# Optimization experiments

Hardware: AMD Instinct MI355X
Metric: run time of the kernel (lower is better)

Reference implementation:

```python
import jax, jax.numpy as jnp
import numpy as np

VOC = 32000
D = 512          # embedding_dim == hidden_dim
POS = 1024       # position_embeddings_count


def _layernorm(x, gamma, beta, eps=1e-5):
    mu = jnp.mean(x, axis=-1, keepdims=True)
    var = jnp.var(x, axis=-1, keepdims=True)
    return (x - mu) * jax.lax.rsqrt(var + eps) * gamma + beta


def setup_inputs() -> dict:
    key = jax.random.key(0)
    ks = jax.random.split(key, 7)
    inp = jax.random.randint(ks[0], (32, 1024), 0, VOC)
    word_emb = jax.random.normal(ks[1], (VOC, D), dtype=jnp.float32) * 0.02
    pos_emb = jax.random.normal(ks[2], (POS, D), dtype=jnp.float32) * 0.02
    gamma = jnp.ones((D,), dtype=jnp.float32)
    beta = jnp.zeros((D,), dtype=jnp.float32)
    # torch.rand -> uniform [0,1) init in the original Attention module
    Wk = jax.random.uniform(ks[3], (D, D), dtype=jnp.float32)
    Wq = jax.random.uniform(ks[4], (D, D), dtype=jnp.float32)
    Wv = jax.random.uniform(ks[5], (D, D), dtype=jnp.float32)
    return {"input": inp, "word_emb": word_emb, "pos_emb": pos_emb,
            "gamma": gamma, "beta": beta, "Wk": Wk, "Wq": Wq, "Wv": Wv}


def reference(input, word_emb, pos_emb, gamma, beta, Wk, Wq, Wv):
    S = input.shape[-1]
    # MiniBertEmbedding: word + positional, then LayerNorm
    emb = word_emb[input] + pos_emb[:S][None, :, :]   # [B,S,D]
    x = _layernorm(emb, gamma, beta)
    # Attention: single-head QK^T softmax V with param matrices
    k = jnp.einsum('bsd,dh->bsh', x, Wk)
    q = jnp.einsum('bsd,dh->bsh', x, Wq)
    v = jnp.einsum('bsd,do->bso', x, Wv)
    qk = jnp.einsum('bqh,bkh->bqk', q, k) / jnp.sqrt(jnp.float32(D))
    attn = jax.nn.softmax(qk, axis=-1)
    return jnp.einsum('bqk,bko->bqo', attn, v)
```

## Files before the change

kernel.cpp:

```cpp
#include <hip/hip_runtime.h>
#include <math.h>

typedef _Float16 f16;
typedef _Float16 half8 __attribute__((ext_vector_type(8)));
typedef _Float16 hv2 __attribute__((ext_vector_type(2)));
typedef _Float16 hv4 __attribute__((ext_vector_type(4)));
typedef float f32x4 __attribute__((ext_vector_type(4)));
typedef __attribute__((address_space(1))) const unsigned int gu32;
typedef __attribute__((address_space(3))) unsigned int lu32;

#define BB 32
#define SS 1024
#define DD 512
#define NR (BB*SS)
#define CH 16

__device__ __forceinline__ void stage128(const char* g, int ldb, char* lds,
                                         int wv, int ln) {
  #pragma unroll
  for (int r = 0; r < 4; r++) {
    int slot = r * 256 + wv * 64 + ln;
    int row = slot >> 3, cp = slot & 7;
    int c = cp ^ (row & 7);
    const char* gp = g + (size_t)row * ldb + (c << 4);
    char* lp = lds + ((slot - ln) << 4);
    __builtin_amdgcn_global_load_lds((gu32*)gp, (lu32*)lp, 16, 0, 0);
  }
}

__device__ __forceinline__ void stage8k_512(const char* g, int ldb, char* lds) {
  int tid = threadIdx.x;
  int slot = tid;
  int row = slot >> 3, cp = slot & 7;
  int c = cp ^ (row & 7);
  const char* gp = g + (size_t)row * ldb + (c << 4);
  char* lp = lds + ((slot - (tid & 63)) << 4);
  __builtin_amdgcn_global_load_lds((gu32*)gp, (lu32*)lp, 16, 0, 0);
}

__device__ __forceinline__ half8 frag_ld(const char* lds, int row, int kc) {
  return *(const half8*)(lds + row * 128 + ((kc ^ (row & 7)) << 4));
}

__device__ __forceinline__ f32x4 MF(half8 a, half8 b, f32x4 c) {
  return __builtin_amdgcn_mfma_f32_16x16x32_f16(a, b, c, 0, 0, 0);
}

__global__ __launch_bounds__(256) void k_prep(
    const int* __restrict__ inp, const float* __restrict__ wemb,
    const float* __restrict__ pemb, const float* __restrict__ gamma,
    const float* __restrict__ beta, f16* __restrict__ Xhi, f16* __restrict__ Xlo,
    const float* __restrict__ Wq, const float* __restrict__ Wk,
    const float* __restrict__ Wv, f16* __restrict__ Wqh, f16* __restrict__ Wql,
    f16* __restrict__ Wkh, f16* __restrict__ Wkl, f16* __restrict__ Wvt)
{
  int bid = blockIdx.x;
  int tid = threadIdx.x;
  __shared__ float red[10];
  __shared__ float Lt[64][65];
  if (bid >= NR) {
    int t  = bid - NR;
    int mz = t >> 6;
    int tt = t & 63;
    if (mz < 2) {
      const float* W = mz ? Wk : Wq;
      f16* Oh = mz ? Wkh : Wqh;
      f16* Ol = mz ? Wkl : Wql;
      #pragma unroll
      for (int p = 0; p < 4; p++) {
        size_t base = (size_t)tt * 4096 + p * 1024 + tid * 4;
        float4 v = *(const float4*)&W[base];
        f16 h0 = (f16)v.x, h1 = (f16)v.y, h2 = (f16)v.z, h3 = (f16)v.w;
        hv4 hi = {h0, h1, h2, h3};
        hv4 lo = {(f16)(v.x - (float)h0), (f16)(v.y - (float)h1),
                  (f16)(v.z - (float)h2), (f16)(v.w - (float)h3)};
        *(hv4*)&Oh[base] = hi;
        *(hv4*)&Ol[base] = lo;
      }
      return;
    }
    int tr = tt >> 3, tc = tt & 7;
    int rr = tid >> 4;
    int c4 = (tid & 15) * 4;
    #pragma unroll
    for (int p = 0; p < 4; p++) {
      float4 v = *(const float4*)&Wv[(size_t)(tr * 64 + p * 16 + rr) * DD + tc * 64 + c4];
      Lt[p * 16 + rr][c4 + 0] = v.x; Lt[p * 16 + rr][c4 + 1] = v.y;
      Lt[p * 16 + rr][c4 + 2] = v.z; Lt[p * 16 + rr][c4 + 3] = v.w;
    }
    __syncthreads();
    #pragma unroll
    for (int p = 0; p < 4; p++) {
      int dl = p * 16 + rr;
      float v0 = Lt[c4 + 0][dl], v1 = Lt[c4 + 1][dl];
      float v2 = Lt[c4 + 2][dl], v3 = Lt[c4 + 3][dl];
      size_t o = (size_t)(tc * 64 + dl) * DD + tr * 64 + c4;
      *(hv4*)&Wvt[o] = (hv4){(f16)v0, (f16)v1, (f16)v2, (f16)v3};
    }
    return;
  }
  int row = bid;
  int s   = row & (SS - 1);
  int tok = inp[row];
  float2 w = ((const float2*)(wemb + (size_t)tok * DD))[tid];
  float2 p = ((const float2*)(pemb + (size_t)s   * DD))[tid];
  float ex = w.x + p.x, ey = w.y + p.y;
  float sum = ex + ey, ssq = ex*ex + ey*ey;
  #pragma unroll
  for (int off = 32; off > 0; off >>= 1) {
    sum += __shfl_down(sum, off, 64);
    ssq += __shfl_down(ssq, off, 64);
  }
  int wv = tid >> 6, ln = tid & 63;
  if (ln == 0) { red[wv] = sum; red[4 + wv] = ssq; }
  __syncthreads();
  if (tid == 0) {
    float s4 = red[0] + red[1] + red[2] + red[3];
    float q4 = red[4] + red[5] + red[6] + red[7];
    float mean = s4 * (1.0f / DD);
    float var  = q4 * (1.0f / DD) - mean * mean;
    red[8] = mean; red[9] = rsqrtf(var + 1e-5f);
  }
  __syncthreads();
  float mean = red[8], rstd = red[9];
  float2 g  = ((const float2*)gamma)[tid];
  float2 bt = ((const float2*)beta)[tid];
  float ox = (ex - mean) * rstd * g.x + bt.x;
  float oy = (ey - mean) * rstd * g.y + bt.y;
  f16 hx = (f16)ox, hy = (f16)oy;
  f16 lx = (f16)(ox - (float)hx), ly = (f16)(oy - (float)hy);
  ((hv2*)(Xhi + (size_t)row * DD))[tid] = (hv2){hx, hy};
  ((hv2*)(Xlo + (size_t)row * DD))[tid] = (hv2){lx, ly};
}

__global__ __launch_bounds__(256, 2) void k_mt(
    const f16* __restrict__ Wkh, const f16* __restrict__ Wkl,
    const f16* __restrict__ Wqh, const f16* __restrict__ Wql,
    f16* __restrict__ Mthi, f16* __restrict__ Mtlo)
{
  __shared__ __align__(16) char Ah[16384], Al[16384], Bh[16384], Bl[16384];
  int tid = threadIdx.x, wv = tid >> 6, ln = tid & 63;
  int mw = wv & 1, nw = wv >> 1;
  int n0 = blockIdx.x * 128;
  int m0 = blockIdx.y * 128;
  f32x4 acc[4][4];
  #pragma unroll
  for (int i = 0; i < 4; i++)
    #pragma unroll
    for (int j = 0; j < 4; j++) acc[i][j] = (f32x4)(0.0f);
  int quad = ln >> 4, l15 = ln & 15;
  for (int k0 = 0; k0 < DD; k0 += 64) {
    __syncthreads();
    stage128((const char*)(Wkh + (size_t)m0 * DD + k0), 1024, Ah, wv, ln);
    stage128((const char*)(Wkl + (size_t)m0 * DD + k0), 1024, Al, wv, ln);
    stage128((const char*)(Wqh + (size_t)n0 * DD + k0), 1024, Bh, wv, ln);
    stage128((const char*)(Wql + (size_t)n0 * DD + k0), 1024, Bl, wv, ln);
    __syncthreads();
    #pragma unroll
    for (int ks = 0; ks < 2; ks++) {
      int kc = ks * 4 + quad;
      half8 ah[4], al[4], bh[4], bl[4];
      #pragma unroll
      for (int t = 0; t < 4; t++) {
        ah[t] = frag_ld(Ah, mw * 64 + t * 16 + l15, kc);
        al[t] = frag_ld(Al, mw * 64 + t * 16 + l15, kc);
        bh[t] = frag_ld(Bh, nw * 64 + t * 16 + l15, kc);
        bl[t] = frag_ld(Bl, nw * 64 + t * 16 + l15, kc);
      }
      #pragma unroll
      for (int i = 0; i < 4; i++)
        #pragma unroll
        for (int j = 0; j < 4; j++) {
          acc[i][j] = MF(ah[i], bh[j], acc[i][j]);
          acc[i][j] = MF(ah[i], bl[j], acc[i][j]);
          acc[i][j] = MF(al[i], bh[j], acc[i][j]);
        }
    }
  }
  #pragma unroll
  for (int i = 0; i < 4; i++)
    #pragma unroll
    for (int j = 0; j < 4; j++)
      #pragma unroll
      for (int rg = 0; rg < 4; rg++) {
        int gm = m0 + mw * 64 + i * 16 + quad * 4 + rg;
        int gn = n0 + nw * 64 + j * 16 + l15;
        size_t o = (size_t)gm * DD + gn;
        float v = acc[i][j][rg];
        f16 h = (f16)v;
        Mthi[o] = h; Mtlo[o] = (f16)(v - (float)h);
      }
}

__global__ __launch_bounds__(256, 2) void k_projm(
    const f16* __restrict__ Xhi, const f16* __restrict__ Xlo,
    const f16* __restrict__ Mthi, const f16* __restrict__ Mtlo,
    f16* __restrict__ Sqhi, f16* __restrict__ Sqlo)
{
  __shared__ __align__(16) char Ah[16384], Al[16384], Bh[16384], Bl[16384];
  int tid = threadIdx.x, wv = tid >> 6, ln = tid & 63;
  int mw = wv & 1, nw = wv >> 1;
  int n0 = blockIdx.x * 128;
  int m0 = blockIdx.y * 128;
  f32x4 acc[4][4];
  #pragma unroll
  for (int i = 0; i < 4; i++)
    #pragma unroll
    for (int j = 0; j < 4; j++) acc[i][j] = (f32x4)(0.0f);
  int quad = ln >> 4, l15 = ln & 15;
  for (int k0 = 0; k0 < DD; k0 += 64) {
    __syncthreads();
    stage128((const char*)(Xhi  + (size_t)m0 * DD + k0), 1024, Ah, wv, ln);
    stage128((const char*)(Xlo  + (size_t)m0 * DD + k0), 1024, Al, wv, ln);
    stage128((const char*)(Mthi + (size_t)n0 * DD + k0), 1024, Bh, wv, ln);
    stage128((const char*)(Mtlo + (size_t)n0 * DD + k0), 1024, Bl, wv, ln);
    __syncthreads();
    #pragma unroll
    for (int ks = 0; ks < 2; ks++) {
      int kc = ks * 4 + quad;
      half8 ah[4], al[4], bh[4], bl[4];
      #pragma unroll
      for (int t = 0; t < 4; t++) {
        ah[t] = frag_ld(Ah, mw * 64 + t * 16 + l15, kc);
        al[t] = frag_ld(Al, mw * 64 + t * 16 + l15, kc);
        bh[t] = frag_ld(Bh, nw * 64 + t * 16 + l15, kc);
        bl[t] = frag_ld(Bl, nw * 64 + t * 16 + l15, kc);
      }
      #pragma unroll
      for (int i = 0; i < 4; i++)
        #pragma unroll
        for (int j = 0; j < 4; j++) {
          acc[i][j] = MF(ah[i], bh[j], acc[i][j]);
          acc[i][j] = MF(ah[i], bl[j], acc[i][j]);
          acc[i][j] = MF(al[i], bh[j], acc[i][j]);
        }
    }
  }
  #pragma unroll
  for (int i = 0; i < 4; i++)
    #pragma unroll
    for (int j = 0; j < 4; j++)
      #pragma unroll
      for (int rg = 0; rg < 4; rg++) {
        int gm = m0 + mw * 64 + i * 16 + quad * 4 + rg;
        int gn = n0 + nw * 64 + j * 16 + l15;
        size_t o = (size_t)gm * DD + gn;
        float v = acc[i][j][rg];
        f16 h = (f16)v;
        Sqhi[o] = h; Sqlo[o] = (f16)(v - (float)h);
      }
}

__global__ __launch_bounds__(256, 2) void k_vt(
    const f16* __restrict__ Wvt, const f16* __restrict__ Xhi, f16* __restrict__ Vt)
{
  __shared__ __align__(16) char Ah[16384], Bh[16384];
  int tid = threadIdx.x, wv = tid >> 6, ln = tid & 63;
  int mw = wv & 1, nw = wv >> 1;
  int n0 = blockIdx.x * 128;
  int m0 = blockIdx.y * 128;
  f32x4 acc[4][4];
  #pragma unroll
  for (int i = 0; i < 4; i++)
    #pragma unroll
    for (int j = 0; j < 4; j++) acc[i][j] = (f32x4)(0.0f);
  for (int k0 = 0; k0 < DD; k0 += 64) {
    __syncthreads();
    stage128((const char*)(Wvt + (size_t)m0 * DD + k0), 1024, Ah, wv, ln);
    stage128((const char*)(Xhi + (size_t)n0 * DD + k0), 1024, Bh, wv, ln);
    __syncthreads();
    int quad = ln >> 4, l15 = ln & 15;
    #pragma unroll
    for (int ks = 0; ks < 2; ks++) {
      int kc = ks * 4 + quad;
      half8 a[4], b[4];
      #pragma unroll
      for (int t = 0; t < 4; t++) {
        a[t] = frag_ld(Ah, mw * 64 + t * 16 + l15, kc);
        b[t] = frag_ld(Bh, nw * 64 + t * 16 + l15, kc);
      }
      #pragma unroll
      for (int i = 0; i < 4; i++)
        #pragma unroll
        for (int j = 0; j < 4; j++) acc[i][j] = MF(a[i], b[j], acc[i][j]);
    }
  }
  int quad = ln >> 4, l15 = ln & 15;
  #pragma unroll
  for (int i = 0; i < 4; i++)
    #pragma unroll
    for (int j = 0; j < 4; j++)
      #pragma unroll
      for (int rg = 0; rg < 4; rg++) {
        int gm = m0 + mw * 64 + i * 16 + quad * 4 + rg;
        int gn = n0 + nw * 64 + j * 16 + l15;
        Vt[(size_t)gm * NR + gn] = (f16)acc[i][j][rg];
      }
}

__global__ __launch_bounds__(512, 2) void k_qk(
    const f16* __restrict__ Sqhi, const f16* __restrict__ Sqlo,
    const f16* __restrict__ Xhi, const f16* __restrict__ Xlo,
    f16* __restrict__ Pws, f16* __restrict__ Pd)
{
  __shared__ __align__(16) char Ah[8192], Al[8192];
  __shared__ __align__(16) char Bh[4][8192], Bl[4][8192];
  __shared__ float redm[4][64], reds[4][64];
  int tid = threadIdx.x, wv = tid >> 6, ln = tid & 63;
  int rowg = wv & 1, qd = wv >> 1;
  int m0 = blockIdx.x * 64;
  int z  = blockIdx.y;
  size_t zr = (size_t)z * SS;
  f32x4 acc[2][16];
  #pragma unroll
  for (int i = 0; i < 2; i++)
    #pragma unroll
    for (int j = 0; j < 16; j++) acc[i][j] = (f32x4)(0.0f);
  int quad = ln >> 4, l15 = ln & 15;

  for (int k0 = 0; k0 < DD; k0 += 64) {
    #pragma unroll
    for (int r = 0; r < 4; r++) {
      __syncthreads();
      if (r == 0) {
        stage8k_512((const char*)(Sqhi + (zr + m0) * DD + k0), 1024, Ah);
        stage8k_512((const char*)(Sqlo + (zr + m0) * DD + k0), 1024, Al);
      }
      #pragma unroll
      for (int q4 = 0; q4 < 4; q4++) {
        int n0 = q4 * 256 + r * 64;
        stage8k_512((const char*)(Xhi + (zr + n0) * DD + k0), 1024, Bh[q4]);
        stage8k_512((const char*)(Xlo + (zr + n0) * DD + k0), 1024, Bl[q4]);
      }
      __syncthreads();
      #pragma unroll
      for (int ks = 0; ks < 2; ks++) {
        int kc = ks * 4 + quad;
        half8 ah[2], al[2];
        #pragma unroll
        for (int i = 0; i < 2; i++) {
          ah[i] = frag_ld(Ah, rowg * 32 + i * 16 + l15, kc);
          al[i] = frag_ld(Al, rowg * 32 + i * 16 + l15, kc);
        }
        #pragma unroll
        for (int jj = 0; jj < 4; jj++) {
          half8 bh = frag_ld(Bh[qd], jj * 16 + l15, kc);
          half8 bl = frag_ld(Bl[qd], jj * 16 + l15, kc);
          #pragma unroll
          for (int i = 0; i < 2; i++) {
            acc[i][r * 4 + jj] = MF(ah[i], bh, acc[i][r * 4 + jj]);
            acc[i][r * 4 + jj] = MF(ah[i], bl, acc[i][r * 4 + jj]);
            acc[i][r * 4 + jj] = MF(al[i], bh, acc[i][r * 4 + jj]);
          }
        }
      }
    }
  }

  const float scale = 0.044194173824159216f;
  float mx[2][4];
  #pragma unroll
  for (int i = 0; i < 2; i++)
    #pragma unroll
    for (int rg = 0; rg < 4; rg++) mx[i][rg] = -3.0e38f;
  #pragma unroll
  for (int i = 0; i < 2; i++)
    #pragma unroll
    for (int j = 0; j < 16; j++)
      #pragma unroll
      for (int rg = 0; rg < 4; rg++) {
        acc[i][j][rg] *= scale;
        mx[i][rg] = fmaxf(mx[i][rg], acc[i][j][rg]);
      }
  #pragma unroll
  for (int off = 1; off < 16; off <<= 1)
    #pragma unroll
    for (int i = 0; i < 2; i++)
      #pragma unroll
      for (int rg = 0; rg < 4; rg++)
        mx[i][rg] = fmaxf(mx[i][rg], __shfl_xor(mx[i][rg], off, 64));
  if (l15 == 0) {
    #pragma unroll
    for (int i = 0; i < 2; i++)
      #pragma unroll
      for (int rg = 0; rg < 4; rg++)
        redm[qd][rowg * 32 + i * 16 + quad * 4 + rg] = mx[i][rg];
  }
  __syncthreads();
  float fm[2][4], sum[2][4];
  #pragma unroll
  for (int i = 0; i < 2; i++)
    #pragma unroll
    for (int rg = 0; rg < 4; rg++) {
      int row = rowg * 32 + i * 16 + quad * 4 + rg;
      fm[i][rg] = fmaxf(fmaxf(redm[0][row], redm[1][row]),
                        fmaxf(redm[2][row], redm[3][row]));
      sum[i][rg] = 0.0f;
    }
  #pragma unroll
  for (int i = 0; i < 2; i++)
    #pragma unroll
    for (int j = 0; j < 16; j++)
      #pragma unroll
      for (int rg = 0; rg < 4; rg++) {
        float e = __expf(acc[i][j][rg] - fm[i][rg]);
        acc[i][j][rg] = e;
        sum[i][rg] += e;
      }
  #pragma unroll
  for (int off = 1; off < 16; off <<= 1)
    #pragma unroll
    for (int i = 0; i < 2; i++)
      #pragma unroll
      for (int rg = 0; rg < 4; rg++)
        sum[i][rg] += __shfl_xor(sum[i][rg], off, 64);
  if (l15 == 0) {
    #pragma unroll
    for (int i = 0; i < 2; i++)
      #pragma unroll
      for (int rg = 0; rg < 4; rg++)
        reds[qd][rowg * 32 + i * 16 + quad * 4 + rg] = sum[i][rg];
  }
  __syncthreads();
  float inv[2][4];
  #pragma unroll
  for (int i = 0; i < 2; i++)
    #pragma unroll
    for (int rg = 0; rg < 4; rg++) {
      int row = rowg * 32 + i * 16 + quad * 4 + rg;
      inv[i][rg] = 1.0f / (reds[0][row] + reds[1][row] + reds[2][row] + reds[3][row]);
    }
  f16* Pb = (z < CH) ? Pws : Pd;
  size_t zo = (size_t)((z < CH) ? z : z - CH);
  #pragma unroll
  for (int i = 0; i < 2; i++)
    #pragma unroll
    for (int j = 0; j < 16; j++)
      #pragma unroll
      for (int rg = 0; rg < 4; rg++) {
        int row = rowg * 32 + i * 16 + quad * 4 + rg;
        int col = qd * 256 + j * 16 + l15;
        Pb[(zo * SS + m0 + row) * SS + col] = (f16)(acc[i][j][rg] * inv[i][rg]);
      }
}

__global__ __launch_bounds__(256, 2) void k_pv(
    const f16* __restrict__ P, const f16* __restrict__ Vt, float* __restrict__ O,
    int zoff)
{
  __shared__ __align__(16) char Ah[16384], Bh[16384];
  int tid = threadIdx.x, wv = tid >> 6, ln = tid & 63;
  int mw = wv & 1, nw = wv >> 1;
  int n0 = blockIdx.x * 128;
  int m0 = blockIdx.y * 128;
  int zl = blockIdx.z;
  int b  = zoff + zl;
  const char* Pt = (const char*)(P + ((size_t)zl * SS + m0) * SS);
  f32x4 acc[4][4];
  #pragma unroll
  for (int i = 0; i < 4; i++)
    #pragma unroll
    for (int j = 0; j < 4; j++) acc[i][j] = (f32x4)(0.0f);
  for (int k0 = 0; k0 < SS; k0 += 64) {
    __syncthreads();
    stage128(Pt + k0 * 2, 2048, Ah, wv, ln);
    stage128((const char*)(Vt + (size_t)n0 * NR + (size_t)b * SS + k0), NR * 2, Bh, wv, ln);
    __syncthreads();
    int quad = ln >> 4, l15 = ln & 15;
    #pragma unroll
    for (int ks = 0; ks < 2; ks++) {
      int kc = ks * 4 + quad;
      half8 a[4], bf[4];
      #pragma unroll
      for (int t = 0; t < 4; t++) {
        a[t]  = frag_ld(Ah, mw * 64 + t * 16 + l15, kc);
        bf[t] = frag_ld(Bh, nw * 64 + t * 16 + l15, kc);
      }
      #pragma unroll
      for (int i = 0; i < 4; i++)
        #pragma unroll
        for (int j = 0; j < 4; j++) acc[i][j] = MF(a[i], bf[j], acc[i][j]);
    }
  }
  int quad = ln >> 4, l15 = ln & 15;
  #pragma unroll
  for (int i = 0; i < 4; i++)
    #pragma unroll
    for (int j = 0; j < 4; j++)
      #pragma unroll
      for (int rg = 0; rg < 4; rg++) {
        int gm = m0 + mw * 64 + i * 16 + quad * 4 + rg;
        int gn = n0 + nw * 64 + j * 16 + l15;
        O[((size_t)b * SS + gm) * DD + gn] = acc[i][j][rg];
      }
}

extern "C" void kernel_launch(void* const* d_in, const int* in_sizes, int n_in,
                              void* d_out, int out_size, void* d_ws, size_t ws_size,
                              hipStream_t stream) {
  const int*   inp   = (const int*)d_in[0];
  const float* wemb  = (const float*)d_in[1];
  const float* pemb  = (const float*)d_in[2];
  const float* gamma = (const float*)d_in[3];
  const float* beta  = (const float*)d_in[4];
  const float* Wk    = (const float*)d_in[5];
  const float* Wq    = (const float*)d_in[6];
  const float* Wv    = (const float*)d_in[7];

  char* ws = (char*)d_ws;
  f16* Xhi  = (f16*)ws;
  f16* Xlo  = (f16*)(ws + ((size_t)32 << 20));
  f16* Sqhi = (f16*)(ws + ((size_t)64 << 20));
  f16* Sqlo = (f16*)(ws + ((size_t)96 << 20));
  f16* Vt   = (f16*)(ws + ((size_t)128 << 20));
  f16* Pws  = (f16*)(ws + ((size_t)160 << 20));
  f16* Pd   = (f16*)d_out;

  f16* Wqh  = (f16*)d_out;
  f16* Wql  = Wqh + (size_t)DD * DD;
  f16* Wkh  = Wql + (size_t)DD * DD;
  f16* Wkl  = Wkh + (size_t)DD * DD;
  f16* Wvt  = Wkl + (size_t)DD * DD;
  f16* Mthi = Wvt + (size_t)DD * DD;
  f16* Mtlo = Mthi + (size_t)DD * DD;

  k_prep<<<NR + 192, 256, 0, stream>>>(inp, wemb, pemb, gamma, beta, Xhi, Xlo,
                                       Wq, Wk, Wv, Wqh, Wql, Wkh, Wkl, Wvt);
  k_mt<<<dim3(DD / 128, DD / 128), 256, 0, stream>>>(Wkh, Wkl, Wqh, Wql, Mthi, Mtlo);
  k_projm<<<dim3(DD / 128, NR / 128), 256, 0, stream>>>(Xhi, Xlo, Mthi, Mtlo, Sqhi, Sqlo);
  k_vt<<<dim3(NR / 128, DD / 128), 256, 0, stream>>>(Wvt, Xhi, Vt);
  k_qk<<<dim3(SS / 64, BB), 512, 0, stream>>>(Sqhi, Sqlo, Xhi, Xlo, Pws, Pd);
  k_pv<<<dim3(DD / 128, SS / 128, CH), 256, 0, stream>>>(Pd,  Vt, (float*)d_out, CH);
  k_pv<<<dim3(DD / 128, SS / 128, CH), 256, 0, stream>>>(Pws, Vt, (float*)d_out, 0);
}
```

Baseline: 466.5 us.

## Double-buffer K-tile staging in k_qk and swizzle block order for locality

The QK^T kernel now double-buffers its key tiles in shared memory. It issues the next tile's global-to-LDS loads before computing on the current one and uses explicit vmcnt waits with raw barriers, instead of two full syncthreads around each synchronous stage. Both k_projm and k_qk now use a flat 1-D grid with a remapped block index, so that groups of 8 consecutive blocks share operand rows or batches, which should improve cache reuse. The doubled B buffers raise k_qk's LDS use to about 144 KB per block, which likely limits it to one block per CU. The hand-written waitcnt counts depend on how many load instructions stage8k_512 emits.

```diff
diff --git a/kernel.cpp b/kernel.cpp
--- a/kernel.cpp
+++ b/kernel.cpp
@@ -200,8 +200,11 @@
   __shared__ __align__(16) char Ah[16384], Al[16384], Bh[16384], Bl[16384];
   int tid = threadIdx.x, wv = tid >> 6, ln = tid & 63;
   int mw = wv & 1, nw = wv >> 1;
-  int n0 = blockIdx.x * 128;
-  int m0 = blockIdx.y * 128;
+  int L = blockIdx.x;
+  int xb = (L >> 3) & 3;
+  int y  = ((L >> 5) << 3) + (L & 7);
+  int n0 = xb * 128;
+  int m0 = y * 128;
   f32x4 acc[4][4];
   #pragma unroll
   for (int i = 0; i < 4; i++)
@@ -304,12 +307,15 @@
     f16* __restrict__ Pws, f16* __restrict__ Pd)
 {
   __shared__ __align__(16) char Ah[8192], Al[8192];
-  __shared__ __align__(16) char Bh[4][8192], Bl[4][8192];
+  __shared__ __align__(16) char Bh[2][4][8192], Bl[2][4][8192];
   __shared__ float redm[4][64], reds[4][64];
   int tid = threadIdx.x, wv = tid >> 6, ln = tid & 63;
   int rowg = wv & 1, qd = wv >> 1;
-  int m0 = blockIdx.x * 64;
-  int z  = blockIdx.y;
+  int L = blockIdx.x;
+  int g  = L >> 7;
+  int rr = L & 127;
+  int z  = g * 8 + (rr & 7);
+  int m0 = (rr >> 3) * 64;
   size_t zr = (size_t)z * SS;
   f32x4 acc[2][16];
   #pragma unroll
@@ -318,21 +324,37 @@
     for (int j = 0; j < 16; j++) acc[i][j] = (f32x4)(0.0f);
   int quad = ln >> 4, l15 = ln & 15;
 
+  #pragma unroll
+  for (int q4 = 0; q4 < 4; q4++) {
+    stage8k_512((const char*)(Xhi + (zr + q4 * 256) * DD), 1024, Bh[0][q4]);
+    stage8k_512((const char*)(Xlo + (zr + q4 * 256) * DD), 1024, Bl[0][q4]);
+  }
+
   for (int k0 = 0; k0 < DD; k0 += 64) {
     #pragma unroll
     for (int r = 0; r < 4; r++) {
-      __syncthreads();
+      __builtin_amdgcn_s_barrier();
+      __builtin_amdgcn_sched_barrier(0);
       if (r == 0) {
         stage8k_512((const char*)(Sqhi + (zr + m0) * DD + k0), 1024, Ah);
         stage8k_512((const char*)(Sqlo + (zr + m0) * DD + k0), 1024, Al);
       }
-      #pragma unroll
-      for (int q4 = 0; q4 < 4; q4++) {
-        int n0 = q4 * 256 + r * 64;
-        stage8k_512((const char*)(Xhi + (zr + n0) * DD + k0), 1024, Bh[q4]);
-        stage8k_512((const char*)(Xlo + (zr + n0) * DD + k0), 1024, Bl[q4]);
-      }
-      __syncthreads();
+      bool haveNext = !(k0 == DD - 64 && r == 3);
+      if (haveNext) {
+        int nk0 = (r == 3) ? k0 + 64 : k0;
+        int nr  = (r + 1) & 3;
+        #pragma unroll
+        for (int q4 = 0; q4 < 4; q4++) {
+          int n0 = q4 * 256 + nr * 64;
+          stage8k_512((const char*)(Xhi + (zr + n0) * DD + nk0), 1024, Bh[(r + 1) & 1][q4]);
+          stage8k_512((const char*)(Xlo + (zr + n0) * DD + nk0), 1024, Bl[(r + 1) & 1][q4]);
+        }
+        asm volatile("s_waitcnt vmcnt(8)" ::: "memory");
+      } else {
+        asm volatile("s_waitcnt vmcnt(0)" ::: "memory");
+      }
+      __builtin_amdgcn_s_barrier();
+      __builtin_amdgcn_sched_barrier(0);
       #pragma unroll
       for (int ks = 0; ks < 2; ks++) {
         int kc = ks * 4 + quad;
@@ -344,8 +366,8 @@
         }
         #pragma unroll
         for (int jj = 0; jj < 4; jj++) {
-          half8 bh = frag_ld(Bh[qd], jj * 16 + l15, kc);
-          half8 bl = frag_ld(Bl[qd], jj * 16 + l15, kc);
+          half8 bh = frag_ld(Bh[r & 1][qd], jj * 16 + l15, kc);
+          half8 bl = frag_ld(Bl[r & 1][qd], jj * 16 + l15, kc);
           #pragma unroll
           for (int i = 0; i < 2; i++) {
             acc[i][r * 4 + jj] = MF(ah[i], bh, acc[i][r * 4 + jj]);
@@ -527,9 +549,9 @@
   k_prep<<<NR + 192, 256, 0, stream>>>(inp, wemb, pemb, gamma, beta, Xhi, Xlo,
                                        Wq, Wk, Wv, Wqh, Wql, Wkh, Wkl, Wvt);
   k_mt<<<dim3(DD / 128, DD / 128), 256, 0, stream>>>(Wkh, Wkl, Wqh, Wql, Mthi, Mtlo);
-  k_projm<<<dim3(DD / 128, NR / 128), 256, 0, stream>>>(Xhi, Xlo, Mthi, Mtlo, Sqhi, Sqlo);
+  k_projm<<<1024, 256, 0, stream>>>(Xhi, Xlo, Mthi, Mtlo, Sqhi, Sqlo);
   k_vt<<<dim3(NR / 128, DD / 128), 256, 0, stream>>>(Wvt, Xhi, Vt);
-  k_qk<<<dim3(SS / 64, BB), 512, 0, stream>>>(Sqhi, Sqlo, Xhi, Xlo, Pws, Pd);
+  k_qk<<<512, 512, 0, stream>>>(Sqhi, Sqlo, Xhi, Xlo, Pws, Pd);
   k_pv<<<dim3(DD / 128, SS / 128, CH), 256, 0, stream>>>(Pd,  Vt, (float*)d_out, CH);
   k_pv<<<dim3(DD / 128, SS / 128, CH), 256, 0, stream>>>(Pws, Vt, (float*)d_out, 0);
 }
```

After: 424.4 us. -9.0%, faster.
